# Kernel tuning notes

Measured on AMD Instinct MI355X. Metric: run time of the kernel, lower is better.

## Reference

```python
import jax, jax.numpy as jnp
import numpy as np

B, T, D, C = 128, 256, 1280, 100


def setup_inputs() -> dict:
    key = jax.random.key(0)
    ks = jax.random.split(key, 6)
    s = 1.0 / np.sqrt(D)  # PyTorch GRU init scale
    return {
        "seq": jax.random.normal(ks[0], (B, T, D), dtype=jnp.float32),
        "candidates": jax.random.normal(ks[1], (B, C, D), dtype=jnp.float32),
        "W_ih": jax.random.normal(ks[2], (3 * D, D), dtype=jnp.float32) * s,
        "W_hh": jax.random.normal(ks[3], (3 * D, D), dtype=jnp.float32) * s,
        "b_ih": jax.random.normal(ks[4], (3 * D,), dtype=jnp.float32) * s,
        "b_hh": jax.random.normal(ks[5], (3 * D,), dtype=jnp.float32) * s,
    }


def _gru_final_hidden(seq, W_ih, W_hh, b_ih, b_hh):
    # seq: [B, T, D]. PyTorch gate order: r, z, n.
    H = W_hh.shape[1]
    # Precompute input projections for all timesteps: [T, B, 3H]
    x_proj = jnp.einsum('btd,gd->tbg', seq, W_ih) + b_ih
    h0 = jnp.zeros((seq.shape[0], H), dtype=seq.dtype)

    def step(h, xp):
        gi_r, gi_z, gi_n = jnp.split(xp, 3, axis=-1)
        gh = h @ W_hh.T + b_hh  # [B, 3H]
        gh_r, gh_z, gh_n = jnp.split(gh, 3, axis=-1)
        r = jax.nn.sigmoid(gi_r + gh_r)
        z = jax.nn.sigmoid(gi_z + gh_z)
        n = jnp.tanh(gi_n + r * gh_n)
        h_new = (1.0 - z) * n + z * h
        return h_new, None

    h_last, _ = jax.lax.scan(step, h0, x_proj)
    return h_last  # [B, H]


def reference(seq, candidates, W_ih, W_hh, b_ih, b_hh):
    hidden = _gru_final_hidden(seq, W_ih, W_hh, b_ih, b_hh)  # [B, D]
    # einsum '...bd,bcd->...bc' with hidden [1,B,D] then squeeze(0) -> [B, C]
    scores = jnp.einsum('bd,bcd->bc', hidden, candidates)
    return scores
```

## Files before the change

### kernel.cpp

```cpp
#include <hip/hip_runtime.h>
#include <hip/hip_bf16.h>

typedef _Float16 f16;
typedef _Float16 f16x8 __attribute__((ext_vector_type(8)));
typedef float f32x4 __attribute__((ext_vector_type(4)));

#define B_ 128
#define T_ 256
#define D_ 1280
#define G3_ 3840
#define C_ 100
#define TB_ 32768
#define NBUF 16

#define O_H16  0ull
#define O_SEQB 0ull
#define O_WIH  83886080ull
#define O_WHH  93716480ull
#define O_XP   103546880ull
#define O_H32  355860480ull
#define O_BAR  356515840ull

__global__ void k_convert(const float* __restrict__ seq, const float* __restrict__ wih,
                          const float* __restrict__ whh, f16* __restrict__ seqb,
                          f16* __restrict__ wih16, f16* __restrict__ whh16,
                          unsigned* __restrict__ bar) {
  if (blockIdx.x == 0) {
    for (int j = threadIdx.x; j < 1024; j += 256)
      __hip_atomic_store(bar + j, 0u, __ATOMIC_RELAXED, __HIP_MEMORY_SCOPE_AGENT);
  }
  const long NSEQ = (long)TB_ * (D_ / 8);
  const long NW = (long)G3_ * (D_ / 8);
  const long total = NSEQ + 2 * NW;
  for (long i = (long)blockIdx.x * blockDim.x + threadIdx.x; i < total;
       i += (long)gridDim.x * blockDim.x) {
    const float* src;
    f16* dst;
    if (i < NSEQ) {
      long row = i / (D_ / 8), c = i % (D_ / 8);
      long t = row >> 7, b = row & 127;
      src = seq + ((b * T_ + t) * (long)D_ + c * 8);
      dst = seqb + (row * (long)D_ + c * 8);
    } else if (i < NSEQ + NW) {
      long j = i - NSEQ;
      src = wih + j * 8;
      dst = wih16 + j * 8;
    } else {
      long j = i - NSEQ - NW;
      src = whh + j * 8;
      dst = whh16 + j * 8;
    }
    float4 a = *(const float4*)src, b4 = *(const float4*)(src + 4);
    f16x8 o;
    o[0] = (f16)a.x; o[1] = (f16)a.y; o[2] = (f16)a.z; o[3] = (f16)a.w;
    o[4] = (f16)b4.x; o[5] = (f16)b4.y; o[6] = (f16)b4.z; o[7] = (f16)b4.w;
    *(f16x8*)dst = o;
  }
}

__device__ __forceinline__ void gl_lds16(const f16* g, f16* lds) {
  __builtin_amdgcn_global_load_lds((const __attribute__((address_space(1))) void*)g,
                                   (__attribute__((address_space(3))) void*)lds, 16, 0, 0);
}

__global__ __launch_bounds__(256) void k_xproj(const f16* __restrict__ A, const f16* __restrict__ Bw,
                                               const float* __restrict__ bih, f16* __restrict__ Cout) {
  __shared__ f16 Alds[128 * 32];
  __shared__ f16 Blds[128 * 32];
  int bid = blockIdx.x;
  int sb = bid / 240;
  int wi = bid % 240;
  int bm = sb * 8 + (wi & 7);
  int bn = wi >> 3;
  long brow = (long)bm * 128;
  int bcol = bn * 128;
  int tid = threadIdx.x, w = tid >> 6, l = tid & 63;
  int wm = w & 1, wn = w >> 1;

  f32x4 acc[4][4] = {};

  int sr = w * 32 + (l >> 2);
  int sc = (l & 3) * 8;
  const f16* gA = A + (brow + sr) * (long)D_ + sc;
  const f16* gB = Bw + (long)(bcol + sr) * D_ + sc;
  f16* lAw = Alds + (w * 32) * 32;
  f16* lBw = Blds + (w * 32) * 32;

  int fr = l & 15, fc = (l >> 4) * 8;

  for (int kb = 0; kb < 40; ++kb) {
    const f16* a0 = gA + kb * 32;
    const f16* b0 = gB + kb * 32;
    gl_lds16(a0, lAw);
    gl_lds16(a0 + 16 * D_, lAw + 16 * 32);
    gl_lds16(b0, lBw);
    gl_lds16(b0 + 16 * D_, lBw + 16 * 32);
    __syncthreads();
    f16x8 af[4], bf[4];
#pragma unroll
    for (int mt = 0; mt < 4; ++mt) af[mt] = *(const f16x8*)(Alds + (wm * 64 + mt * 16 + fr) * 32 + fc);
#pragma unroll
    for (int nt = 0; nt < 4; ++nt) bf[nt] = *(const f16x8*)(Blds + (wn * 64 + nt * 16 + fr) * 32 + fc);
#pragma unroll
    for (int mt = 0; mt < 4; ++mt)
#pragma unroll
      for (int nt = 0; nt < 4; ++nt)
        acc[mt][nt] = __builtin_amdgcn_mfma_f32_16x16x32_f16(af[mt], bf[nt], acc[mt][nt], 0, 0, 0);
    __syncthreads();
  }
#pragma unroll
  for (int nt = 0; nt < 4; ++nt) {
    int col = bcol + wn * 64 + nt * 16 + fr;
    int g = col / D_;
    int dcol = col - g * D_;
    int cg = dcol >> 4, c16 = dcol & 15;
    float bv = bih[col];
    f16* base = Cout + (((long)bm * 80 + cg) * 3 + g) * 2048 + c16;
#pragma unroll
    for (int mt = 0; mt < 4; ++mt) {
#pragma unroll
      for (int i = 0; i < 4; ++i) {
        int b = wm * 64 + mt * 16 + (l >> 4) * 4 + i;
        base[b * 16] = (f16)(acc[mt][nt][i] + bv);
      }
    }
  }
}

__global__ __launch_bounds__(256, 1) void k_scan(const f16* __restrict__ whh16,
                                                 const f16* __restrict__ xproj,
                                                 const float* __restrict__ bhh,
                                                 f16* __restrict__ h16, float* __restrict__ h32,
                                                 unsigned* __restrict__ bar) {
  __shared__ f16 wlds[3 * 16 * D_];
  int wg = blockIdx.x;
  int rg = (wg & 7) >> 2;
  int q = wg >> 3;
  int cg = q * 4 + (wg & 3);
  int r0 = rg * 64, d0 = cg * 16;
  int tid = threadIdx.x, w = tid >> 6, l = tid & 63;
  int wr0 = r0 + w * 16;
  int fr = l & 15, fq = l >> 4;
  int mycol = d0 + fr;
  int shard = ((q & 3) << 2) | (wg & 3);
  unsigned* mycnt = bar + (rg * 16 + shard) * 32;
  int koff = (q & 3) * 10;

  for (int qq = tid; qq < 3 * 16 * 160; qq += 256) {
    int rowg = qq / 160, c8 = qq % 160;
    int g = rowg >> 4, j = rowg & 15;
    int kb = c8 >> 2, kq = c8 & 3;
    uint4 v = *(const uint4*)(whh16 + ((long)(g * D_ + d0 + j)) * D_ + c8 * 8);
    *(uint4*)(wlds + (((kb * 3 + g) * 4 + kq) * 16 + j) * 8) = v;
  }
#pragma unroll
  for (int i = 0; i < 4; ++i) {
    if ((fr & 1) == 0) {
      unsigned* p = (unsigned*)(h16 + (wr0 + fq * 4 + i) * D_ + mycol);
      __hip_atomic_store(p, 0u, __ATOMIC_RELAXED, __HIP_MEMORY_SCOPE_AGENT);
    }
  }

  float bh0 = bhh[0 * D_ + mycol];
  float bh1 = bhh[1 * D_ + mycol];
  float bh2 = bhh[2 * D_ + mycol];
  float hreg[4] = {0.f, 0.f, 0.f, 0.f};
  f16 xg0[4], xg1[4], xg2[4];

  auto prefetch_x = [&](int tt) {
    const f16* xs = xproj + (((long)tt * 80 + cg) * 3) * 2048 + fr;
#pragma unroll
    for (int i = 0; i < 4; ++i) {
      int b = wr0 + fq * 4 + i;
      xg0[i] = xs[0 * 2048 + b * 16];
      xg1[i] = xs[1 * 2048 + b * 16];
      xg2[i] = xs[2 * 2048 + b * 16];
    }
  };
  auto poll16 = [&](unsigned target) {
    unsigned it = 0;
    for (;;) {
      unsigned v = target;
      if (l < 16)
        v = __hip_atomic_load(bar + (rg * 16 + l) * 32, __ATOMIC_RELAXED, __HIP_MEMORY_SCOPE_AGENT);
      if (__all(v >= target)) break;
      __builtin_amdgcn_s_sleep(1);
      if (++it > 500000u) {
        if (l < 16)
          v = __hip_atomic_fetch_add(bar + (rg * 16 + l) * 32, 0u, __ATOMIC_RELAXED,
                                     __HIP_MEMORY_SCOPE_AGENT);
        if (__all(v >= target)) break;
        it = 0;
      }
    }
  };

  prefetch_x(0);

  __syncthreads();
  if (tid == 0)
    __hip_atomic_fetch_add(mycnt, 1u, __ATOMIC_RELAXED, __HIP_MEMORY_SCOPE_AGENT);
  if (tid < 64) {
    poll16(5u);
    if (tid == 0) __builtin_amdgcn_fence(__ATOMIC_ACQUIRE, "agent");
  }
  __syncthreads();

  unsigned tgt = 10u;
  for (int t = 0; t < T_; ++t) {
    const f16* hc = h16 + (t & (NBUF - 1)) * (B_ * D_);
    const f16* arow = hc + (wr0 + fr) * (long)D_ + fq * 8;
    f32x4 acc0 = {}, acc1 = {}, acc2 = {};
#pragma unroll 10
    for (int ii = 0; ii < 40; ++ii) {
      int kb = ii + koff;
      kb = (kb >= 40) ? kb - 40 : kb;
      f16x8 a = *(const f16x8*)(arow + kb * 32);
      const f16* wb = wlds + kb * 1536 + (fq * 16 + fr) * 8;
      f16x8 b0 = *(const f16x8*)(wb);
      f16x8 b1 = *(const f16x8*)(wb + 512);
      f16x8 b2 = *(const f16x8*)(wb + 1024);
      acc0 = __builtin_amdgcn_mfma_f32_16x16x32_f16(a, b0, acc0, 0, 0, 0);
      acc1 = __builtin_amdgcn_mfma_f32_16x16x32_f16(a, b1, acc1, 0, 0, 0);
      acc2 = __builtin_amdgcn_mfma_f32_16x16x32_f16(a, b2, acc2, 0, 0, 0);
    }
    float hnew[4];
#pragma unroll
    for (int i = 0; i < 4; ++i) {
      float gr = (float)xg0[i], gz = (float)xg1[i], gn = (float)xg2[i];
      float r = 1.f / (1.f + __expf(-(gr + acc0[i] + bh0)));
      float z = 1.f / (1.f + __expf(-(gz + acc1[i] + bh1)));
      float pn = gn + r * (acc2[i] + bh2);
      pn = fminf(fmaxf(pn, -30.f), 30.f);
      float e = __expf(-2.f * pn);
      float n = (1.f - e) / (1.f + e);
      hnew[i] = (1.f - z) * n + z * hreg[i];
      hreg[i] = hnew[i];
    }
    if (t == T_ - 1) break;
    f16* hn = h16 + ((t + 1) & (NBUF - 1)) * (B_ * D_);
#pragma unroll
    for (int i = 0; i < 4; ++i) {
      int row = wr0 + fq * 4 + i;
      unsigned short bits = __builtin_bit_cast(unsigned short, (f16)hnew[i]);
      unsigned other = (unsigned)__shfl_xor((int)bits, 1);
      if ((fr & 1) == 0) {
        unsigned val = (unsigned)bits | (other << 16);
        unsigned* p = (unsigned*)(hn + row * D_ + mycol);
        __hip_atomic_store(p, val, __ATOMIC_RELAXED, __HIP_MEMORY_SCOPE_AGENT);
      }
    }
    __syncthreads();
    if (tid == 0)
      __hip_atomic_fetch_add(mycnt, 1u, __ATOMIC_RELAXED, __HIP_MEMORY_SCOPE_AGENT);
    prefetch_x(t + 1);
    if (tid < 64) {
      poll16(tgt);
      if (tid == 0 && (((t + 1) & (NBUF - 1)) == 0))
        __builtin_amdgcn_fence(__ATOMIC_ACQUIRE, "agent");
    }
    __syncthreads();
    tgt += 5u;
  }
#pragma unroll
  for (int i = 0; i < 4; ++i) h32[(wr0 + fq * 4 + i) * D_ + mycol] = hreg[i];
}

__global__ __launch_bounds__(256) void k_scores(const float* __restrict__ h32,
                                                const float* __restrict__ cand,
                                                float* __restrict__ out) {
  int gw = blockIdx.x * 4 + (threadIdx.x >> 6);
  int l = threadIdx.x & 63;
  int b = gw / C_, c = gw % C_;
  const float* hp = h32 + (long)b * D_;
  const float* cp = cand + ((long)b * C_ + c) * D_;
  float s = 0.f;
#pragma unroll
  for (int q = 0; q < 5; ++q) {
    int d = q * 256 + l * 4;
    float4 hv = *(const float4*)(hp + d);
    float4 cv = *(const float4*)(cp + d);
    s += hv.x * cv.x + hv.y * cv.y + hv.z * cv.z + hv.w * cv.w;
  }
#pragma unroll
  for (int off = 32; off > 0; off >>= 1) s += __shfl_down(s, off);
  if (l == 0) out[(long)b * C_ + c] = s;
}

extern "C" void kernel_launch(void* const* d_in, const int* in_sizes, int n_in, void* d_out,
                              int out_size, void* d_ws, size_t ws_size, hipStream_t stream) {
  const float* seq = (const float*)d_in[0];
  const float* cand = (const float*)d_in[1];
  const float* wih = (const float*)d_in[2];
  const float* whh = (const float*)d_in[3];
  const float* bih = (const float*)d_in[4];
  const float* bhh = (const float*)d_in[5];
  char* ws = (char*)d_ws;
  f16* seqb = (f16*)(ws + O_SEQB);
  f16* wih16 = (f16*)(ws + O_WIH);
  f16* whh16 = (f16*)(ws + O_WHH);
  f16* xp = (f16*)(ws + O_XP);
  f16* h16 = (f16*)(ws + O_H16);
  float* h32 = (float*)(ws + O_H32);
  unsigned* bar = (unsigned*)(ws + O_BAR);

  k_convert<<<2048, 256, 0, stream>>>(seq, wih, whh, seqb, wih16, whh16, bar);
  k_xproj<<<7680, 256, 0, stream>>>(seqb, wih16, bih, xp);
  k_scan<<<160, 256, 0, stream>>>(whh16, xp, bhh, h16, h32, bar);
  k_scores<<<3200, 256, 0, stream>>>(h32, cand, (float*)d_out);
}
```

Measured before the change: 2.276 ms.

## Split GRU scan over 640 blocks with register-resident W_hh and split-K LDS reduction

The recurrent scan now launches 640 workgroups instead of 160. Each covers 16 batch rows by 16 hidden columns, and its four waves split the K dimension, with W_hh fragments held in registers instead of LDS. Partial MFMA sums are reduced through a small swizzled LDS buffer, and each thread applies the GRU gates for one element. The aim is more parallelism per timestep and shorter per-step latency. In exchange, each row group's barrier now polls 40 counters instead of 16, register pressure rises, and all 640 blocks must be co-resident for the spin barrier to work.

```diff
diff --git a/kernel.cpp b/kernel.cpp
--- a/kernel.cpp
+++ b/kernel.cpp
@@ -26,7 +26,7 @@
                           f16* __restrict__ wih16, f16* __restrict__ whh16,
                           unsigned* __restrict__ bar) {
   if (blockIdx.x == 0) {
-    for (int j = threadIdx.x; j < 1024; j += 256)
+    for (int j = threadIdx.x; j < 10240; j += 256)
       __hip_atomic_store(bar + j, 0u, __ATOMIC_RELAXED, __HIP_MEMORY_SCOPE_AGENT);
   }
   const long NSEQ = (long)TB_ * (D_ / 8);
@@ -127,67 +127,56 @@
   }
 }
 
-__global__ __launch_bounds__(256, 1) void k_scan(const f16* __restrict__ whh16,
+__global__ __launch_bounds__(256, 3) void k_scan(const f16* __restrict__ whh16,
                                                  const f16* __restrict__ xproj,
                                                  const float* __restrict__ bhh,
                                                  f16* __restrict__ h16, float* __restrict__ h32,
                                                  unsigned* __restrict__ bar) {
-  __shared__ f16 wlds[3 * 16 * D_];
+  __shared__ float red[4][3][256];
   int wg = blockIdx.x;
-  int rg = (wg & 7) >> 2;
-  int q = wg >> 3;
-  int cg = q * 4 + (wg & 3);
-  int r0 = rg * 64, d0 = cg * 16;
+  int rg = wg & 7, cg = wg >> 3;
+  int r0 = rg * 16, d0 = cg * 16;
   int tid = threadIdx.x, w = tid >> 6, l = tid & 63;
-  int wr0 = r0 + w * 16;
   int fr = l & 15, fq = l >> 4;
-  int mycol = d0 + fr;
-  int shard = ((q & 3) << 2) | (wg & 3);
-  unsigned* mycnt = bar + (rg * 16 + shard) * 32;
-  int koff = (q & 3) * 10;
-
-  for (int qq = tid; qq < 3 * 16 * 160; qq += 256) {
-    int rowg = qq / 160, c8 = qq % 160;
-    int g = rowg >> 4, j = rowg & 15;
-    int kb = c8 >> 2, kq = c8 & 3;
-    uint4 v = *(const uint4*)(whh16 + ((long)(g * D_ + d0 + j)) * D_ + c8 * 8);
-    *(uint4*)(wlds + (((kb * 3 + g) * 4 + kq) * 16 + j) * 8) = v;
-  }
-#pragma unroll
-  for (int i = 0; i < 4; ++i) {
-    if ((fr & 1) == 0) {
-      unsigned* p = (unsigned*)(h16 + (wr0 + fq * 4 + i) * D_ + mycol);
-      __hip_atomic_store(p, 0u, __ATOMIC_RELAXED, __HIP_MEMORY_SCOPE_AGENT);
-    }
-  }
-
-  float bh0 = bhh[0 * D_ + mycol];
-  float bh1 = bhh[1 * D_ + mycol];
-  float bh2 = bhh[2 * D_ + mycol];
-  float hreg[4] = {0.f, 0.f, 0.f, 0.f};
-  f16 xg0[4], xg1[4], xg2[4];
+  int erow = tid >> 4, ecol = tid & 15;
+  unsigned* mycnt = bar + (rg * 40 + (cg % 40)) * 32;
+
+  const f16* wbase = whh16 + (long)(d0 + fr) * D_ + w * 320 + fq * 8;
+  f16x8 wf[10][3];
+#pragma unroll
+  for (int j = 0; j < 10; ++j)
+#pragma unroll
+    for (int g = 0; g < 3; ++g)
+      wf[j][g] = *(const f16x8*)(wbase + (long)g * (D_ * D_) + j * 32);
+
+  if ((tid & 1) == 0) {
+    unsigned* p = (unsigned*)(h16 + (r0 + erow) * D_ + d0 + ecol);
+    __hip_atomic_store(p, 0u, __ATOMIC_RELAXED, __HIP_MEMORY_SCOPE_AGENT);
+  }
+
+  float bh0 = bhh[0 * D_ + d0 + ecol];
+  float bh1 = bhh[1 * D_ + d0 + ecol];
+  float bh2 = bhh[2 * D_ + d0 + ecol];
+  float hreg = 0.f;
+  f16 xr, xz, xn;
 
   auto prefetch_x = [&](int tt) {
-    const f16* xs = xproj + (((long)tt * 80 + cg) * 3) * 2048 + fr;
-#pragma unroll
-    for (int i = 0; i < 4; ++i) {
-      int b = wr0 + fq * 4 + i;
-      xg0[i] = xs[0 * 2048 + b * 16];
-      xg1[i] = xs[1 * 2048 + b * 16];
-      xg2[i] = xs[2 * 2048 + b * 16];
-    }
+    const f16* xs = xproj + (((long)tt * 80 + cg) * 3) * 2048 + (r0 + erow) * 16 + ecol;
+    xr = xs[0];
+    xz = xs[2048];
+    xn = xs[4096];
   };
-  auto poll16 = [&](unsigned target) {
+  auto poll = [&](unsigned target) {
     unsigned it = 0;
     for (;;) {
       unsigned v = target;
-      if (l < 16)
-        v = __hip_atomic_load(bar + (rg * 16 + l) * 32, __ATOMIC_RELAXED, __HIP_MEMORY_SCOPE_AGENT);
+      if (l < 40)
+        v = __hip_atomic_load(bar + (rg * 40 + l) * 32, __ATOMIC_RELAXED, __HIP_MEMORY_SCOPE_AGENT);
       if (__all(v >= target)) break;
       __builtin_amdgcn_s_sleep(1);
       if (++it > 500000u) {
-        if (l < 16)
-          v = __hip_atomic_fetch_add(bar + (rg * 16 + l) * 32, 0u, __ATOMIC_RELAXED,
+        if (l < 40)
+          v = __hip_atomic_fetch_add(bar + (rg * 40 + l) * 32, 0u, __ATOMIC_RELAXED,
                                      __HIP_MEMORY_SCOPE_AGENT);
         if (__all(v >= target)) break;
         it = 0;
@@ -201,69 +190,65 @@
   if (tid == 0)
     __hip_atomic_fetch_add(mycnt, 1u, __ATOMIC_RELAXED, __HIP_MEMORY_SCOPE_AGENT);
   if (tid < 64) {
-    poll16(5u);
+    poll(2u);
     if (tid == 0) __builtin_amdgcn_fence(__ATOMIC_ACQUIRE, "agent");
   }
   __syncthreads();
 
-  unsigned tgt = 10u;
+  const f16* abase = (const f16*)h16 + (long)(r0 + fr) * D_ + w * 320 + fq * 8;
+  unsigned tgt = 4u;
   for (int t = 0; t < T_; ++t) {
-    const f16* hc = h16 + (t & (NBUF - 1)) * (B_ * D_);
-    const f16* arow = hc + (wr0 + fr) * (long)D_ + fq * 8;
+    const f16* arow = abase + (long)(t & (NBUF - 1)) * (B_ * D_);
     f32x4 acc0 = {}, acc1 = {}, acc2 = {};
-#pragma unroll 10
-    for (int ii = 0; ii < 40; ++ii) {
-      int kb = ii + koff;
-      kb = (kb >= 40) ? kb - 40 : kb;
-      f16x8 a = *(const f16x8*)(arow + kb * 32);
-      const f16* wb = wlds + kb * 1536 + (fq * 16 + fr) * 8;
-      f16x8 b0 = *(const f16x8*)(wb);
-      f16x8 b1 = *(const f16x8*)(wb + 512);
-      f16x8 b2 = *(const f16x8*)(wb + 1024);
-      acc0 = __builtin_amdgcn_mfma_f32_16x16x32_f16(a, b0, acc0, 0, 0, 0);
-      acc1 = __builtin_amdgcn_mfma_f32_16x16x32_f16(a, b1, acc1, 0, 0, 0);
-      acc2 = __builtin_amdgcn_mfma_f32_16x16x32_f16(a, b2, acc2, 0, 0, 0);
-    }
-    float hnew[4];
+#pragma unroll
+    for (int j = 0; j < 10; ++j) {
+      f16x8 a = *(const f16x8*)(arow + j * 32);
+      acc0 = __builtin_amdgcn_mfma_f32_16x16x32_f16(a, wf[j][0], acc0, 0, 0, 0);
+      acc1 = __builtin_amdgcn_mfma_f32_16x16x32_f16(a, wf[j][1], acc1, 0, 0, 0);
+      acc2 = __builtin_amdgcn_mfma_f32_16x16x32_f16(a, wf[j][2], acc2, 0, 0, 0);
+    }
 #pragma unroll
     for (int i = 0; i < 4; ++i) {
-      float gr = (float)xg0[i], gz = (float)xg1[i], gn = (float)xg2[i];
-      float r = 1.f / (1.f + __expf(-(gr + acc0[i] + bh0)));
-      float z = 1.f / (1.f + __expf(-(gz + acc1[i] + bh1)));
-      float pn = gn + r * (acc2[i] + bh2);
-      pn = fminf(fmaxf(pn, -30.f), 30.f);
-      float e = __expf(-2.f * pn);
-      float n = (1.f - e) / (1.f + e);
-      hnew[i] = (1.f - z) * n + z * hreg[i];
-      hreg[i] = hnew[i];
-    }
+      int pos = (((fq * 4 + i) * 16) + fr) ^ (fq << 2);
+      red[w][0][pos] = acc0[i];
+      red[w][1][pos] = acc1[i];
+      red[w][2][pos] = acc2[i];
+    }
+    __syncthreads();
+    int pr = tid ^ ((tid >> 6) << 2);
+    float s0 = red[0][0][pr] + red[1][0][pr] + red[2][0][pr] + red[3][0][pr];
+    float s1 = red[0][1][pr] + red[1][1][pr] + red[2][1][pr] + red[3][1][pr];
+    float s2 = red[0][2][pr] + red[1][2][pr] + red[2][2][pr] + red[3][2][pr];
+    float r = 1.f / (1.f + __expf(-((float)xr + s0 + bh0)));
+    float z = 1.f / (1.f + __expf(-((float)xz + s1 + bh1)));
+    float pn = (float)xn + r * (s2 + bh2);
+    pn = fminf(fmaxf(pn, -30.f), 30.f);
+    float e2 = __expf(-2.f * pn);
+    float nn = (1.f - e2) / (1.f + e2);
+    float hv = (1.f - z) * nn + z * hreg;
+    hreg = hv;
     if (t == T_ - 1) break;
-    f16* hn = h16 + ((t + 1) & (NBUF - 1)) * (B_ * D_);
-#pragma unroll
-    for (int i = 0; i < 4; ++i) {
-      int row = wr0 + fq * 4 + i;
-      unsigned short bits = __builtin_bit_cast(unsigned short, (f16)hnew[i]);
-      unsigned other = (unsigned)__shfl_xor((int)bits, 1);
-      if ((fr & 1) == 0) {
-        unsigned val = (unsigned)bits | (other << 16);
-        unsigned* p = (unsigned*)(hn + row * D_ + mycol);
-        __hip_atomic_store(p, val, __ATOMIC_RELAXED, __HIP_MEMORY_SCOPE_AGENT);
-      }
+    unsigned short bits = __builtin_bit_cast(unsigned short, (f16)hv);
+    unsigned other = (unsigned)__shfl_xor((int)bits, 1);
+    if ((tid & 1) == 0) {
+      unsigned val = (unsigned)bits | (other << 16);
+      f16* hn = h16 + (long)((t + 1) & (NBUF - 1)) * (B_ * D_);
+      __hip_atomic_store((unsigned*)(hn + (r0 + erow) * D_ + d0 + ecol), val, __ATOMIC_RELAXED,
+                         __HIP_MEMORY_SCOPE_AGENT);
     }
     __syncthreads();
     if (tid == 0)
       __hip_atomic_fetch_add(mycnt, 1u, __ATOMIC_RELAXED, __HIP_MEMORY_SCOPE_AGENT);
     prefetch_x(t + 1);
     if (tid < 64) {
-      poll16(tgt);
+      poll(tgt);
       if (tid == 0 && (((t + 1) & (NBUF - 1)) == 0))
         __builtin_amdgcn_fence(__ATOMIC_ACQUIRE, "agent");
     }
     __syncthreads();
-    tgt += 5u;
-  }
-#pragma unroll
-  for (int i = 0; i < 4; ++i) h32[(wr0 + fq * 4 + i) * D_ + mycol] = hreg[i];
+    tgt += 2u;
+  }
+  h32[(r0 + erow) * D_ + d0 + ecol] = hreg;
 }
 
 __global__ __launch_bounds__(256) void k_scores(const float* __restrict__ h32,
@@ -306,6 +291,6 @@
 
   k_convert<<<2048, 256, 0, stream>>>(seq, wih, whh, seqb, wih16, whh16, bar);
   k_xproj<<<7680, 256, 0, stream>>>(seqb, wih16, bih, xp);
-  k_scan<<<160, 256, 0, stream>>>(whh16, xp, bhh, h16, h32, bar);
+  k_scan<<<640, 256, 0, stream>>>(whh16, xp, bhh, h16, h32, bar);
   k_scores<<<3200, 256, 0, stream>>>(h32, cand, (float*)d_out);
 }
```

Result: slower. 2.396 ms (+5.3%).
